# Optimization experiments

Hardware: AMD Instinct MI355X
Metric: run time of the kernel (lower is better)

## Reference

```python
import jax, jax.numpy as jnp
import numpy as np

B, N, D, H = 2, 4096, 512, 8
HD = D // H

def setup_inputs() -> dict:
    key = jax.random.key(0)
    ks = jax.random.split(key, 5)
    s = 1.0 / np.sqrt(D)
    return {
        "x": jax.random.normal(ks[0], (B, N, D), dtype=jnp.float32),
        "W_qkv": jax.random.uniform(ks[1], (D, 3 * D), minval=-s, maxval=s, dtype=jnp.float32),
        "b_qkv": jax.random.uniform(ks[2], (3 * D,), minval=-s, maxval=s, dtype=jnp.float32),
        "W_out": jax.random.uniform(ks[3], (D, D), minval=-s, maxval=s, dtype=jnp.float32),
        "b_out": jax.random.uniform(ks[4], (D,), minval=-s, maxval=s, dtype=jnp.float32),
    }

def reference(x, W_qkv, b_qkv, W_out, b_out):
    Bq, Nq, Dq = x.shape
    scale = HD ** -0.5
    qkv = x @ W_qkv + b_qkv                      # [B,N,3D]
    qkv = qkv.reshape(Bq, Nq, 3, H, HD)
    q, k, v = (jnp.moveaxis(qkv[:, :, i], 2, 1) for i in range(3))  # [B,H,N,hd]
    attn = jnp.einsum('bhqd,bhkd->bhqk', q, k) * scale   # [B,H,N,N]
    causal = jnp.tril(jnp.ones((Nq, Nq), dtype=bool))
    attn = jnp.where(causal, attn, -jnp.inf)
    attn = jax.nn.softmax(attn, axis=-1)
    out = jnp.einsum('bhqk,bhkd->bhqd', attn, v)         # [B,H,N,hd]
    out = jnp.moveaxis(out, 1, 2).reshape(Bq, Nq, Dq)
    return out @ W_out + b_out
```

## Files before the change

### kernel.cpp

```cpp
#include <hip/hip_runtime.h>
#include <hip/hip_bf16.h>


typedef __bf16 bf16_t;
typedef __bf16 bf16x4 __attribute__((ext_vector_type(4)));
typedef __bf16 bf16x8 __attribute__((ext_vector_type(8)));
typedef float  f32x4  __attribute__((ext_vector_type(4)));

__device__ __forceinline__ void gload_lds16(const bf16_t* g, bf16_t* l) {
    __builtin_amdgcn_global_load_lds(
        (const __attribute__((address_space(1))) void*)g,
        (__attribute__((address_space(3))) void*)l, 16, 0, 0);
}


__global__ void convert_f32_bf16(const float* __restrict__ in, bf16_t* __restrict__ out) {
    int i = blockIdx.x * 256 + threadIdx.x;
    float4 v = ((const float4*)in)[i];
    bf16x4 o;
    o[0] = (bf16_t)v.x; o[1] = (bf16_t)v.y; o[2] = (bf16_t)v.z; o[3] = (bf16_t)v.w;
    ((bf16x4*)out)[i] = o;
}

__global__ void transpose_tiled(const float* __restrict__ in, bf16_t* __restrict__ out, int N) {
    __shared__ bf16_t T[64][72];
    const int tid = threadIdx.x;
    const int n0 = blockIdx.x * 64, k0 = blockIdx.y * 64;
    #pragma unroll
    for (int pass = 0; pass < 4; ++pass) {
        int kk = pass * 16 + (tid >> 4), nn = (tid & 15) * 4;
        float4 v = *(const float4*)(in + (size_t)(k0 + kk) * N + n0 + nn);
        T[nn + 0][kk] = (bf16_t)v.x; T[nn + 1][kk] = (bf16_t)v.y;
        T[nn + 2][kk] = (bf16_t)v.z; T[nn + 3][kk] = (bf16_t)v.w;
    }
    __syncthreads();
    #pragma unroll
    for (int pass = 0; pass < 2; ++pass) {
        int n = pass * 32 + (tid >> 3), c8 = (tid & 7) * 8;
        *(bf16x8*)(out + (size_t)(n0 + n) * 512 + k0 + c8) = *(const bf16x8*)&T[n][c8];
    }
}

__global__ void transpose_v(const bf16_t* __restrict__ Vg, bf16_t* __restrict__ Vt) {
    __shared__ bf16_t T[64 * 64];
    const int tid = threadIdx.x;
    const int bh = blockIdx.x >> 6, n0 = (blockIdx.x & 63) * 64;
    const bf16_t* src = Vg + ((size_t)bh * 4096 + n0) * 64;
    #pragma unroll
    for (int i = 0; i < 2; ++i) {
        int c = tid + i * 256, n = c >> 3, h8 = (c & 7) * 8;
        bf16x8 v = *(const bf16x8*)(src + (size_t)n * 64 + h8);
        const int swz = (n >> 3) ^ (h8 >> 3);
        bf16_t* base = &T[swz * 8 + (n & 7)];
        #pragma unroll
        for (int j = 0; j < 8; ++j) base[(h8 + j) * 64] = v[j];
    }
    __syncthreads();
    bf16_t* dst = Vt + (size_t)bh * 64 * 4096 + n0;
    #pragma unroll
    for (int i = 0; i < 2; ++i) {
        int c = tid + i * 256, hd = c >> 3, cn = c & 7;
        *(bf16x8*)(dst + (size_t)hd * 4096 + cn * 8) =
            *(const bf16x8*)&T[hd * 64 + ((cn ^ (hd >> 3)) * 8)];
    }
}


template <int MODE, int TN>
__global__ __launch_bounds__(256) void gemm_bt(
    const bf16_t* __restrict__ A, const bf16_t* __restrict__ Bt,
    const float* __restrict__ bias,
    bf16_t* __restrict__ Qg, bf16_t* __restrict__ Kg, bf16_t* __restrict__ Vg,
    float* __restrict__ Cout)
{
    constexpr int NI = (TN == 128) ? 4 : 2;
    __shared__ bf16_t As[128 * 64];
    __shared__ bf16_t Bs[TN * 64];
    const int tid  = threadIdx.x;
    const int wid  = tid >> 6, lane = tid & 63, l16 = lane & 15, quad = lane >> 4;
    const int l8   = l16 & 7;
    const int wr   = (TN == 128) ? (wid >> 1) * 64 : wid * 32;
    const int wc   = (TN == 128) ? (wid & 1) * 64 : 0;
    const int m0   = blockIdx.y * 128, n0 = blockIdx.x * TN;

    f32x4 acc[NI][4] = {};

    for (int kk = 0; kk < 512; kk += 64) {
        __syncthreads();
        #pragma unroll
        for (int i = 0; i < 4; ++i) {
            int slot = tid + i * 256;
            int row = slot >> 3, cg = (slot & 7) ^ (row & 7);
            gload_lds16(A + (size_t)(m0 + row) * 512 + kk + cg * 8,
                        (bf16_t*)((char*)As + ((i * 256 + (wid << 6)) << 4)));
        }
        #pragma unroll
        for (int i = 0; i < TN / 32; ++i) {
            int slot = tid + i * 256;
            int row = slot >> 3, cg = (slot & 7) ^ (row & 7);
            gload_lds16(Bt + (size_t)(n0 + row) * 512 + kk + cg * 8,
                        (bf16_t*)((char*)Bs + ((i * 256 + (wid << 6)) << 4)));
        }
        __syncthreads();
        #pragma unroll
        for (int s = 0; s < 2; ++s) {
            const int sw = (s * 4 + quad);
            bf16x8 a[NI], b[4];
            #pragma unroll
            for (int i = 0; i < NI; ++i) {
                int row = wr + i * 16 + l16;
                a[i] = *(const bf16x8*)&As[(row * 8 + (sw ^ l8)) * 8];
            }
            #pragma unroll
            for (int j = 0; j < 4; ++j) {
                int row = wc + j * 16 + l16;
                b[j] = *(const bf16x8*)&Bs[(row * 8 + (sw ^ l8)) * 8];
            }
            #pragma unroll
            for (int i = 0; i < NI; ++i)
                #pragma unroll
                for (int j = 0; j < 4; ++j)
                    acc[i][j] = __builtin_amdgcn_mfma_f32_16x16x32_bf16(a[i], b[j], acc[i][j], 0, 0, 0);
        }
    }

    const float qscale = 0.18033688011112042f;
    #pragma unroll
    for (int i = 0; i < NI; ++i) {
        int mrow = m0 + wr + i * 16 + quad * 4;
        #pragma unroll
        for (int j = 0; j < 4; ++j) {
            int cgl = n0 + wc + j * 16 + l16;
            float bv = bias[cgl];
            #pragma unroll
            for (int r = 0; r < 4; ++r) {
                int m = mrow + r;
                float val = acc[i][j][r] + bv;
                if (MODE == 0) {
                    int which = cgl >> 9, hh = (cgl >> 6) & 7, hd = cgl & 63;
                    int b_ = m >> 12, n = m & 4095, bh = b_ * 8 + hh;
                    size_t idx = ((size_t)bh * 4096 + n) * 64 + hd;
                    if (which == 0)      Qg[idx] = (bf16_t)(val * qscale);
                    else if (which == 1) Kg[idx] = (bf16_t)val;
                    else                 Vg[idx] = (bf16_t)val;
                } else {
                    Cout[(size_t)m * 512 + cgl] = val;
                }
            }
        }
    }
}


__global__ __launch_bounds__(256, 3) void attn_ns2(
    const bf16_t* __restrict__ Qg, const bf16_t* __restrict__ Kg,
    const bf16_t* __restrict__ Vt,
    float* __restrict__ o_part, float* __restrict__ l_part, int nsplit)
{
    __shared__ bf16_t Ks[2][64][72];
    __shared__ bf16_t Vs[2][64][72];
    __shared__ bf16_t Ps[4][16][72];

    const int tid  = threadIdx.x;
    const int w    = tid >> 6, lane = tid & 63, l16 = lane & 15, quad = lane >> 4;
    const int bh   = blockIdx.x & 15, pr = (blockIdx.x >> 4) & 15, h = blockIdx.x >> 8;

    float* ob = o_part + (size_t)(h * 16 + bh) * 4096 * 64;
    float* lb = l_part + (size_t)(h * 16 + bh) * 4096;

    const int srow = tid >> 3, scol = (tid & 7) * 8;
    const int srow1 = srow + 32;
    const float MSHIFT = 12.0f;

    bf16x8 ones;
    #pragma unroll
    for (int j = 0; j < 8; ++j) ones[j] = (bf16_t)1.0f;

    uint4 kr0, kr1, vr0, vr1;

    for (int ph = 0; ph < 2; ++ph) {
        const int st = ph ? (31 - pr) : pr;
        const int T  = 2 * st + 2;
        const int b0 = (h * T) / nsplit, b1 = ((h + 1) * T) / nsplit;

        int qrow[2];
        bf16x8 qf[2][2];
        #pragma unroll
        for (int s = 0; s < 2; ++s) {
            qrow[s] = st * 128 + s * 64 + w * 16 + l16;
            const bf16_t* qp = Qg + ((size_t)bh * 4096 + qrow[s]) * 64;
            qf[s][0] = *(const bf16x8*)(qp + quad * 8);
            qf[s][1] = *(const bf16x8*)(qp + 32 + quad * 8);
        }

        f32x4 o[2][4] = {};
        f32x4 lacc[2] = {};

        {
            const size_t kb = ((size_t)bh * 4096 + b0 * 64) * 64;
            const size_t vb = (size_t)bh * 64 * 4096 + b0 * 64;
            kr0 = *(const uint4*)(Kg + kb + (size_t)srow * 64 + scol);
            kr1 = *(const uint4*)(Kg + kb + (size_t)srow1 * 64 + scol);
            vr0 = *(const uint4*)(Vt + vb + (size_t)srow * 4096 + scol);
            vr1 = *(const uint4*)(Vt + vb + (size_t)srow1 * 4096 + scol);
        }
        __syncthreads();

        for (int kt = b0; kt < b1; ++kt) {
            const int cur = kt & 1;
            *(uint4*)&Ks[cur][srow][scol]  = kr0;
            *(uint4*)&Ks[cur][srow1][scol] = kr1;
            *(uint4*)&Vs[cur][srow][scol]  = vr0;
            *(uint4*)&Vs[cur][srow1][scol] = vr1;
            __syncthreads();

            if (kt + 1 < b1) {
                const size_t kb = ((size_t)bh * 4096 + (kt + 1) * 64) * 64;
                const size_t vb = (size_t)bh * 64 * 4096 + (kt + 1) * 64;
                kr0 = *(const uint4*)(Kg + kb + (size_t)srow * 64 + scol);
                kr1 = *(const uint4*)(Kg + kb + (size_t)srow1 * 64 + scol);
                vr0 = *(const uint4*)(Vt + vb + (size_t)srow * 4096 + scol);
                vr1 = *(const uint4*)(Vt + vb + (size_t)srow1 * 4096 + scol);
            }

            bf16x8 kf[4][2], vf[4][2];
            #pragma unroll
            for (int cb = 0; cb < 4; ++cb) {
                kf[cb][0] = *(const bf16x8*)&Ks[cur][cb * 16 + l16][quad * 8];
                kf[cb][1] = *(const bf16x8*)&Ks[cur][cb * 16 + l16][32 + quad * 8];
            }
            #pragma unroll
            for (int j = 0; j < 4; ++j) {
                vf[j][0] = *(const bf16x8*)&Vs[cur][j * 16 + l16][quad * 8];
                vf[j][1] = *(const bf16x8*)&Vs[cur][j * 16 + l16][32 + quad * 8];
            }

            #pragma unroll
            for (int s = 0; s < 2; ++s) {
                const int diag = 2 * st + s;
                if (kt > diag) continue;

                f32x4 sv[4] = {};
                #pragma unroll
                for (int cb = 0; cb < 4; ++cb) {
                    sv[cb] = __builtin_amdgcn_mfma_f32_16x16x32_bf16(kf[cb][0], qf[s][0], sv[cb], 0, 0, 0);
                    sv[cb] = __builtin_amdgcn_mfma_f32_16x16x32_bf16(kf[cb][1], qf[s][1], sv[cb], 0, 0, 0);
                }

                if (kt == diag) {
                    #pragma unroll
                    for (int cb = 0; cb < 4; ++cb) {
                        const int keyg = kt * 64 + cb * 16 + quad * 4;
                        #pragma unroll
                        for (int r = 0; r < 4; ++r)
                            if (keyg + r > qrow[s]) sv[cb][r] = -1e30f;
                    }
                }

                #pragma unroll
                for (int cb = 0; cb < 4; ++cb) {
                    bf16x4 pk;
                    #pragma unroll
                    for (int r = 0; r < 4; ++r)
                        pk[r] = (bf16_t)__builtin_amdgcn_exp2f(sv[cb][r] - MSHIFT);
                    *(bf16x4*)&Ps[w][l16][cb * 16 + quad * 4] = pk;
                }
                bf16x8 pa0 = *(const bf16x8*)&Ps[w][l16][quad * 8];
                bf16x8 pa1 = *(const bf16x8*)&Ps[w][l16][32 + quad * 8];

                #pragma unroll
                for (int j = 0; j < 4; ++j) {
                    o[s][j] = __builtin_amdgcn_mfma_f32_16x16x32_bf16(pa0, vf[j][0], o[s][j], 0, 0, 0);
                    o[s][j] = __builtin_amdgcn_mfma_f32_16x16x32_bf16(pa1, vf[j][1], o[s][j], 0, 0, 0);
                }
                lacc[s] = __builtin_amdgcn_mfma_f32_16x16x32_bf16(pa0, ones, lacc[s], 0, 0, 0);
                lacc[s] = __builtin_amdgcn_mfma_f32_16x16x32_bf16(pa1, ones, lacc[s], 0, 0, 0);
            }
        }

        #pragma unroll
        for (int s = 0; s < 2; ++s)
            #pragma unroll
            for (int r = 0; r < 4; ++r) {
                int n = st * 128 + s * 64 + w * 16 + quad * 4 + r;
                #pragma unroll
                for (int j = 0; j < 4; ++j)
                    ob[(size_t)n * 64 + j * 16 + l16] = o[s][j][r];
                if (l16 == 0) lb[n] = lacc[s][r];
            }
    }
}

__global__ void combine_kernel(const float* __restrict__ o_part,
                               const float* __restrict__ l_part,
                               bf16_t* __restrict__ Og, int ns)
{
    int t = blockIdx.x * 256 + threadIdx.x;
    int oct = t & 7, n = (t >> 3) & 4095, bh = t >> 15;
    size_t base = ((size_t)bh * 4096 + n) * 64 + oct * 8;
    f32x4 s0 = {}, s1 = {};
    float l = 0.f;
    for (int h = 0; h < ns; ++h) {
        const float* op = o_part + (size_t)h * 16 * 4096 * 64 + base;
        s0 += *(const f32x4*)op;
        s1 += *(const f32x4*)(op + 4);
        l  += l_part[(size_t)h * 16 * 4096 + (size_t)bh * 4096 + n];
    }
    float inv = 1.0f / l;
    bf16x8 res;
    #pragma unroll
    for (int j = 0; j < 4; ++j) {
        res[j]     = (bf16_t)(s0[j] * inv);
        res[j + 4] = (bf16_t)(s1[j] * inv);
    }
    *(bf16x8*)(Og + ((size_t)((bh >> 3) * 4096 + n)) * 512 + (bh & 7) * 64 + oct * 8) = res;
}


extern "C" void kernel_launch(void* const* d_in, const int* in_sizes, int n_in,
                              void* d_out, int out_size, void* d_ws, size_t ws_size,
                              hipStream_t stream) {
    const float* x    = (const float*)d_in[0];
    const float* Wqkv = (const float*)d_in[1];
    const float* bqkv = (const float*)d_in[2];
    const float* Wout = (const float*)d_in[3];
    const float* bout = (const float*)d_in[4];
    float* out = (float*)d_out;

    char* ws = (char*)d_ws;
    bf16_t* xb  = (bf16_t*)(ws);
    bf16_t* WqT = (bf16_t*)(ws + 8388608);
    bf16_t* WoT = (bf16_t*)(ws + 9961472);
    bf16_t* Qg  = (bf16_t*)(ws + 10485760);
    bf16_t* Kg  = (bf16_t*)(ws + 18874368);
    bf16_t* Vt  = (bf16_t*)(ws + 27262976);
    bf16_t* Vg  = (bf16_t*)(ws + 35651584);

    const int nsplit = (ws_size >= 86769664ULL) ? 3 : 2;
    float* o_part = (float*)(ws + 35651584);
    float* l_part = (float*)(ws + 35651584 + (size_t)nsplit * 16777216);

    convert_f32_bf16<<<4096, 256, 0, stream>>>(x, xb);
    transpose_tiled<<<dim3(24, 8), 256, 0, stream>>>(Wqkv, WqT, 1536);
    transpose_tiled<<<dim3(8, 8), 256, 0, stream>>>(Wout, WoT, 512);

    gemm_bt<0, 128><<<dim3(12, 64), 256, 0, stream>>>(xb, WqT, bqkv, Qg, Kg, Vg, nullptr);
    transpose_v<<<1024, 256, 0, stream>>>(Vg, Vt);

    attn_ns2<<<256 * nsplit, 256, 0, stream>>>(Qg, Kg, Vt, o_part, l_part, nsplit);
    combine_kernel<<<2048, 256, 0, stream>>>(o_part, l_part, xb , nsplit);

    gemm_bt<1, 64><<<dim3(8, 64), 256, 0, stream>>>(xb, WoT, bout, nullptr, nullptr, nullptr, out);
}
```

Baseline: 190.0 us.

## Repack P via permlane swaps instead of LDS and raise occupancy/split

The softmax probabilities used to make a round trip through per-wave LDS. They are now rearranged from the score-MFMA output layout into the PV-MFMA A-operand layout in registers, using permlane32/permlane16 swaps. This removes the LDS write/read and its latency from the inner attention loop and frees shared memory. Launch bounds go from 3 to 4 blocks per SIMD, and the key split count can rise to 4 when the workspace is large enough. The trade-offs are more register pressure and more partial-combine traffic when the split is 4.

```diff
diff --git a/kernel.cpp b/kernel.cpp
--- a/kernel.cpp
+++ b/kernel.cpp
@@ -3,9 +3,11 @@
 
 
 typedef __bf16 bf16_t;
+typedef __bf16 bf16x2 __attribute__((ext_vector_type(2)));
 typedef __bf16 bf16x4 __attribute__((ext_vector_type(4)));
 typedef __bf16 bf16x8 __attribute__((ext_vector_type(8)));
 typedef float  f32x4  __attribute__((ext_vector_type(4)));
+typedef unsigned int uint32x4 __attribute__((ext_vector_type(4)));
 
 __device__ __forceinline__ void gload_lds16(const bf16_t* g, bf16_t* l) {
     __builtin_amdgcn_global_load_lds(
@@ -152,14 +154,13 @@
 }
 
 
-__global__ __launch_bounds__(256, 3) void attn_ns2(
+__global__ __launch_bounds__(256, 4) void attn_ns2(
     const bf16_t* __restrict__ Qg, const bf16_t* __restrict__ Kg,
     const bf16_t* __restrict__ Vt,
     float* __restrict__ o_part, float* __restrict__ l_part, int nsplit)
 {
     __shared__ bf16_t Ks[2][64][72];
     __shared__ bf16_t Vs[2][64][72];
-    __shared__ bf16_t Ps[4][16][72];
 
     const int tid  = threadIdx.x;
     const int w    = tid >> 6, lane = tid & 63, l16 = lane & 15, quad = lane >> 4;
@@ -257,16 +258,32 @@
                     }
                 }
 
+                unsigned int c[4][2];
                 #pragma unroll
                 for (int cb = 0; cb < 4; ++cb) {
-                    bf16x4 pk;
                     #pragma unroll
-                    for (int r = 0; r < 4; ++r)
-                        pk[r] = (bf16_t)__builtin_amdgcn_exp2f(sv[cb][r] - MSHIFT);
-                    *(bf16x4*)&Ps[w][l16][cb * 16 + quad * 4] = pk;
-                }
-                bf16x8 pa0 = *(const bf16x8*)&Ps[w][l16][quad * 8];
-                bf16x8 pa1 = *(const bf16x8*)&Ps[w][l16][32 + quad * 8];
+                    for (int t = 0; t < 2; ++t) {
+                        bf16x2 pk2;
+                        pk2[0] = (bf16_t)__builtin_amdgcn_exp2f(sv[cb][2 * t]     - MSHIFT);
+                        pk2[1] = (bf16_t)__builtin_amdgcn_exp2f(sv[cb][2 * t + 1] - MSHIFT);
+                        c[cb][t] = __builtin_bit_cast(unsigned int, pk2);
+                    }
+                }
+
+                unsigned int pw0[4], pw1[4];
+                #pragma unroll
+                for (int t = 0; t < 2; ++t) {
+                    auto u  = __builtin_amdgcn_permlane32_swap(c[0][t], c[1][t], false, false);
+                    auto z  = __builtin_amdgcn_permlane16_swap(u[0], u[1], false, false);
+                    pw0[t] = z[0]; pw0[t + 2] = z[1];
+                    auto u2 = __builtin_amdgcn_permlane32_swap(c[2][t], c[3][t], false, false);
+                    auto z2 = __builtin_amdgcn_permlane16_swap(u2[0], u2[1], false, false);
+                    pw1[t] = z2[0]; pw1[t + 2] = z2[1];
+                }
+                uint32x4 w0v = {pw0[0], pw0[1], pw0[2], pw0[3]};
+                uint32x4 w1v = {pw1[0], pw1[1], pw1[2], pw1[3]};
+                bf16x8 pa0 = __builtin_bit_cast(bf16x8, w0v);
+                bf16x8 pa1 = __builtin_bit_cast(bf16x8, w1v);
 
                 #pragma unroll
                 for (int j = 0; j < 4; ++j) {
@@ -336,7 +353,8 @@
     bf16_t* Vt  = (bf16_t*)(ws + 27262976);
     bf16_t* Vg  = (bf16_t*)(ws + 35651584);
 
-    const int nsplit = (ws_size >= 86769664ULL) ? 3 : 2;
+    const int nsplit = (ws_size >= 103809024ULL) ? 4
+                     : (ws_size >= 86769664ULL)  ? 3 : 2;
     float* o_part = (float*)(ws + 35651584);
     float* l_part = (float*)(ws + 35651584 + (size_t)nsplit * 16777216);
 
```

Result: slower. 393.0 us (+106.9%).
